# Optimization experiments

Measured on AMD Instinct MI355X. Metric: run time of the kernel, lower is better.

Reference implementation:

```python
import jax, jax.numpy as jnp
import numpy as np

K_SIZE = 5
SIGMA_IMG = 0.2
SIGMA_VGG = 0.02
BN_EPS = 1e-5
NORM = 2.0  # 2 * len(GPU_IDS), assuming 1 device


def _window_shifts(x, k):
    # x: (n, C, H, W) -> (n, C, H, W, k*k) neighbor values for every offset in
    # the k x k window, zero-padded at image borders.
    r = k // 2
    n, C, H, W = x.shape
    xp = jnp.pad(x, ((0, 0), (0, 0), (r, r), (r, r)))
    cols = [xp[:, :, di:di + H, dj:dj + W] for di in range(k) for dj in range(k)]
    return jnp.stack(cols, axis=-1)


def _modularity(img, seg, k, sigma):
    # img: (n, C, H, W) feature map; seg: (n, K, H, W) soft assignments.
    n, K, H, W = seg.shape
    seg2 = _window_shifts(seg, k)                                  # (n,K,H,W,kk)
    img2 = _window_shifts(img, k)                                  # (n,C,H,W,kk)
    valid = _window_shifts(jnp.ones((1, 1, H, W), img.dtype), k)[:, 0]  # (1,H,W,kk)
    d2 = ((img[..., None] - img2) ** 2).sum(axis=1)                # (n,H,W,kk)
    w12 = jax.lax.stop_gradient(jnp.exp(-d2 / (2.0 * sigma * sigma)) * valid)
    # numerator: sum over pixels & pairs of p1*p2*w12, per (n, K)
    num = jnp.einsum('nkhw,nkhwp,nhwp->nk', seg, seg2, w12)
    # p1 (sum over pairs of p1/n_pairs) == seg; w1 = sum over pairs of w12
    w1 = w12.sum(axis=-1)                                          # (n,H,W)
    den = jnp.einsum('nhw,nkhw->nk', w1, seg)
    rel = num / den                                                # (n,K)
    return rel.sum(axis=1) / (K * n)                               # (n,)


def _conv(x, w, b):
    y = jax.lax.conv_general_dilated(x, w, (1, 1), 'SAME',
                                     dimension_numbers=('NCHW', 'OIHW', 'NCHW'))
    return y + b[None, :, None, None]


def _maxpool2(x):
    return jax.lax.reduce_window(x, -jnp.inf, jax.lax.max,
                                 (1, 1, 2, 2), (1, 1, 2, 2), 'VALID')


def _avgpool2(x):
    n, c, h, w = x.shape
    return x.reshape(n, c, h // 2, 2, w // 2, 2).mean(axis=(3, 5))


def _vgg8(x, w1, b1, w2, b2, w3, b3, w4, b4):
    # VGG16 features[:8]: conv1_1, conv1_2, maxpool, conv2_1, conv2_2 (relu each)
    x = jax.nn.relu(_conv(x, w1, b1))
    x = jax.nn.relu(_conv(x, w2, b2))
    x = _maxpool2(x)
    x = jax.nn.relu(_conv(x, w3, b3))
    x = jax.nn.relu(_conv(x, w4, b4))
    return x


def _batchnorm(x):
    # fresh BatchNorm2d in training mode (weight=1, bias=0), then detach
    m = x.mean(axis=(0, 2, 3), keepdims=True)
    v = x.var(axis=(0, 2, 3), keepdims=True)
    return jax.lax.stop_gradient((x - m) / jnp.sqrt(v + BN_EPS))


def setup_inputs() -> dict:
    key = jax.random.key(0)
    ks = jax.random.split(key, 6)
    images = jax.random.uniform(ks[0], (4, 3, 128, 128), jnp.float32)
    seg = jax.random.uniform(ks[1], (4, 8, 128, 128), jnp.float32)
    segmentation = seg / seg.sum(axis=1, keepdims=True)
    w1 = jax.random.normal(ks[2], (64, 3, 3, 3), jnp.float32) * 0.1
    w2 = jax.random.normal(ks[3], (64, 64, 3, 3), jnp.float32) * 0.05
    w3 = jax.random.normal(ks[4], (128, 64, 3, 3), jnp.float32) * 0.05
    w4 = jax.random.normal(ks[5], (128, 128, 3, 3), jnp.float32) * 0.03
    return {'images': images, 'segmentation': segmentation,
            'w1': w1, 'b1': jnp.zeros(64), 'w2': w2, 'b2': jnp.zeros(64),
            'w3': w3, 'b3': jnp.zeros(128), 'w4': w4, 'b4': jnp.zeros(128)}


def reference(images, segmentation, w1, b1, w2, b2, w3, b3, w4, b4):
    fich = _batchnorm(_vgg8(images, w1, b1, w2, b2, w3, b3, w4, b4))  # (n,128,64,64)
    images_n = _batchnorm(images)
    down_seg = segmentation
    while down_seg.shape[-1] != fich.shape[-1]:
        down_seg = _avgpool2(down_seg)
    loss = (_modularity(fich, down_seg, K_SIZE, SIGMA_VGG).sum()
            + _modularity(images_n, segmentation, K_SIZE, SIGMA_IMG).sum())
    return loss / NORM
```

## Files before the change

kernel.cpp:

```cpp
#include <hip/hip_runtime.h>
#include <hip/hip_bf16.h>
#include <math.h>

typedef __attribute__((ext_vector_type(8))) short short8;
typedef __attribute__((ext_vector_type(4))) float floatx4;
typedef unsigned short ushortT;

__device__ inline short f2bf(float v) {
    __hip_bfloat16 h = __float2bfloat16(v);
    union { __hip_bfloat16 h; short s; } u; u.h = h; return u.s;
}

#define OFF_C2    0
#define OFF_PAD4  8388608
#define OFF_FICH  12849152
#define OFF_PAD2  21237760
#define OFF_PAD3  29890560
#define OFF_WP2   32120832
#define OFF_WP3   32194560
#define OFF_WP4   32342016
#define OFF_ST    33947648
#define OFF_P64   33951744
#define OFF_P128  33968128
#define OFF_PBN   34033664
#define OFF_PIMG  34295808

__global__ __launch_bounds__(256) void prologue(
    char* ws, const float* __restrict__ images,
    const float* __restrict__ w1, const float* __restrict__ b1,
    const float* __restrict__ w2, const float* __restrict__ w3,
    const float* __restrict__ w4)
{
    __shared__ float plds[3 * 720];
    __shared__ float rs[256], rs2[256];

    int b = blockIdx.x;
    int tid = threadIdx.x;

    if (b >= 1362) {
        int bid = b - 1362;
        int txt = bid & 7; bid >>= 3;
        int tyt = bid & 7; bid >>= 3;
        int ocg = bid & 7; bid >>= 3;
        int n = bid;
        int x0 = txt * 16, y0 = tyt * 16;
        int tx = tid & 15, ty = tid >> 4;
        short* outp = (short*)(ws + OFF_PAD2);

        for (int i = tid; i < 972; i += 256) {
            int cc = i / 324; int rem = i - cc * 324;
            int r = rem / 18, c = rem - r * 18;
            int y = y0 - 1 + r, x = x0 - 1 + c;
            float v = 0.f;
            if ((unsigned)y < 128u && (unsigned)x < 128u)
                v = images[((size_t)(n * 3 + cc) * 128 + y) * 128 + x];
            plds[cc * 720 + r * 40 + c] = v;
        }
        __syncthreads();

        float acc[8];
#pragma unroll
        for (int oc = 0; oc < 8; ++oc) acc[oc] = 0.f;
        const float* w_g = w1 + (size_t)(ocg * 8) * 27;
#pragma unroll
        for (int cc = 0; cc < 3; ++cc) {
            const float* base = &plds[cc * 720 + ty * 40 + tx];
            float i00 = base[0],  i01 = base[1],  i02 = base[2];
            float i10 = base[40], i11 = base[41], i12 = base[42];
            float i20 = base[80], i21 = base[81], i22 = base[82];
            const float* wp = w_g + cc * 9;
#pragma unroll
            for (int oc = 0; oc < 8; ++oc) {
                const float* wq = wp + oc * 27;
                float a = acc[oc];
                a = fmaf(wq[0], i00, a); a = fmaf(wq[1], i01, a); a = fmaf(wq[2], i02, a);
                a = fmaf(wq[3], i10, a); a = fmaf(wq[4], i11, a); a = fmaf(wq[5], i12, a);
                a = fmaf(wq[6], i20, a); a = fmaf(wq[7], i21, a); a = fmaf(wq[8], i22, a);
                acc[oc] = a;
            }
        }
        int oy = y0 + ty, ox = x0 + tx;
        short* o = outp + ((size_t)(n * 130 + oy + 1) * 130 + ox + 1) * 64 + ocg * 8;
#pragma unroll
        for (int oc = 0; oc < 8; ++oc) {
            float v = fmaxf(acc[oc] + b1[ocg * 8 + oc], 0.f);
            o[oc] = f2bf(v);
        }
        return;
    }

    if (b < 162) {
        int t = b * 256 + tid;
        short* base; int Hp, Wp, C; int idx;
        if (t < 16512)      { base = (short*)(ws + OFF_PAD2); Hp = 130; Wp = 130; C = 64;  idx = t; }
        else if (t < 24832) { base = (short*)(ws + OFF_PAD3); Hp = 66;  Wp = 66;  C = 64;  idx = t - 16512; }
        else if (t < 41472) { base = (short*)(ws + OFF_PAD4); Hp = 66;  Wp = 66;  C = 128; idx = t - 24832; }
        else return;
        int c8 = idx % (C / 8); int rest = idx / (C / 8);
        int haloPx = 2 * Wp + 2 * (Hp - 2);
        int p = rest % haloPx; int n = rest / haloPx;
        int y, x;
        if (p < Wp)          { y = 0;      x = p; }
        else if (p < 2 * Wp) { y = Hp - 1; x = p - Wp; }
        else { int j = p - 2 * Wp; y = 1 + (j >> 1); x = (j & 1) ? (Wp - 1) : 0; }
        short8 z = {0, 0, 0, 0, 0, 0, 0, 0};
        *(short8*)&base[((size_t)((n * Hp + y) * Wp) + x) * C + c8 * 8] = z;
        return;
    }
    if (b < 1170) {
        int e = (b - 162) * 256 + tid;
        const float* w; short* wp; int CIN, NTALL;
        if (e < 36864)       { w = w2; wp = (short*)(ws + OFF_WP2); CIN = 64;  NTALL = 4; }
        else if (e < 110592) { e -= 36864;  w = w3; wp = (short*)(ws + OFF_WP3); CIN = 64;  NTALL = 8; }
        else if (e < 258048) { e -= 110592; w = w4; wp = (short*)(ws + OFF_WP4); CIN = 128; NTALL = 8; }
        else return;
        int j = e & 7; int L = (e >> 3) & 63; int rest = e >> 9;
        int nt = rest % NTALL; int rest2 = rest / NTALL;
        int KT = CIN / 32;
        int kt = rest2 % KT; int t = rest2 / KT;
        int oc = nt * 16 + (L & 15);
        int ci = kt * 32 + (L >> 4) * 8 + j;
        wp[e] = f2bf(w[((size_t)oc * CIN + ci) * 9 + t]);
        return;
    }
    {
        float* part = (float*)(ws + OFF_PIMG);
        int bb = b - 1170;
        int c = bb >> 6, chunk = bb & 63;
        int base = chunk * 1024 + tid;
        float s = 0.f, s2 = 0.f;
#pragma unroll
        for (int k = 0; k < 4; ++k) {
            int i = base + k * 256;
            int n = i >> 14, hw = i & 16383;
            float v = images[(((size_t)(n * 3 + c)) << 14) + hw];
            s += v; s2 = fmaf(v, v, s2);
        }
        rs[tid] = s; rs2[tid] = s2;
        __syncthreads();
        for (int k = 128; k > 0; k >>= 1) {
            if (tid < k) { rs[tid] += rs[tid + k]; rs2[tid] += rs2[tid + k]; }
            __syncthreads();
        }
        if (tid == 0) { part[bb * 2] = rs[0]; part[bb * 2 + 1] = rs2[0]; }
    }
}

__global__ __launch_bounds__(256) void conv2_pool(
    const short* __restrict__ inp,
    const short* __restrict__ wp,
    const float* __restrict__ bias,
    short* __restrict__ outp)
{
    constexpr int CIN = 64;
    constexpr int Hp = 130, Wp = 130;

    int bid = blockIdx.x;
    int o2 = bid & 1; bid >>= 1;
    int xt = bid & 1; bid >>= 1;
    int yq = bid & 31; bid >>= 5;
    int n = bid;
    int y0 = yq * 4;
    int x0 = xt * 64;

    int tid = threadIdx.x;
    int wv = tid >> 6, lane = tid & 63;
    int lm = lane & 15, q = lane >> 4;
    int px0 = x0 + 16 * wv;
    int ntb = o2 * 2;

    floatx4 acc[4][2];
#pragma unroll
    for (int d = 0; d < 4; ++d)
#pragma unroll
        for (int t = 0; t < 2; ++t) acc[d][t] = (floatx4){0.f, 0.f, 0.f, 0.f};

    const short* a_m = inp + lm * CIN + q * 8;
    const short* wbase = wp + ((size_t)ntb * 64 + lane) * 8;

    for (int kt = 0; kt < 2; ++kt) {
        int kofs = kt * 32;
#pragma unroll
        for (int s = 0; s < 3; ++s) {
            const short* acol = a_m + ((size_t)((n * Hp + y0) * Wp) + px0 + s) * CIN + kofs;
            short8 av[6];
#pragma unroll
            for (int j = 0; j < 6; ++j)
                av[j] = *(const short8*)(acol + (size_t)j * Wp * CIN);
#pragma unroll
            for (int r = 0; r < 3; ++r) {
                const short* bp = wbase + (size_t)(((r * 3 + s) * 2 + kt) * 4) * 512;
                short8 b0 = *(const short8*)bp;
                short8 b1 = *(const short8*)(bp + 512);
#pragma unroll
                for (int d = 0; d < 4; ++d) {
                    acc[d][0] = __builtin_amdgcn_mfma_f32_16x16x32_bf16(av[r + d], b0, acc[d][0], 0, 0, 0);
                    acc[d][1] = __builtin_amdgcn_mfma_f32_16x16x32_bf16(av[r + d], b1, acc[d][1], 0, 0, 0);
                }
            }
        }
    }

    int ox = (px0 + q * 4) >> 1;
#pragma unroll
    for (int t2 = 0; t2 < 2; ++t2) {
        int oc = (ntb + t2) * 16 + lm;
        float bs = bias[oc];
#pragma unroll
        for (int p = 0; p < 2; ++p) {
            float v00 = fmaxf(acc[2 * p][t2][0] + bs, 0.f);
            float v01 = fmaxf(acc[2 * p][t2][1] + bs, 0.f);
            float v02 = fmaxf(acc[2 * p][t2][2] + bs, 0.f);
            float v03 = fmaxf(acc[2 * p][t2][3] + bs, 0.f);
            float v10 = fmaxf(acc[2 * p + 1][t2][0] + bs, 0.f);
            float v11 = fmaxf(acc[2 * p + 1][t2][1] + bs, 0.f);
            float v12 = fmaxf(acc[2 * p + 1][t2][2] + bs, 0.f);
            float v13 = fmaxf(acc[2 * p + 1][t2][3] + bs, 0.f);
            float m0 = fmaxf(fmaxf(v00, v01), fmaxf(v10, v11));
            float m1 = fmaxf(fmaxf(v02, v03), fmaxf(v12, v13));
            int oy = yq * 2 + p;
            short* o = outp + ((size_t)(n * 66 + oy + 1) * 66 + ox + 1) * 64 + oc;
            o[0]  = f2bf(m0);
            o[64] = f2bf(m1);
        }
    }
}

__device__ __forceinline__ void mod128_body(
    int obid,
    const float* __restrict__ img, const float* __restrict__ pimg,
    const float* __restrict__ seg, float* __restrict__ part,
    float (*il)[12][4], float (*sl)[12][14], float* stm)
{
    int t = threadIdx.x;
    int w = t >> 6, lane = t & 63;
    int tx = lane & 7, ty = lane >> 3;

    if (t < 64) {
#pragma unroll
        for (int ch = 0; ch < 3; ++ch) {
            float s  = pimg[(ch * 64 + t) * 2];
            float s2 = pimg[(ch * 64 + t) * 2 + 1];
#pragma unroll
            for (int sh = 32; sh > 0; sh >>= 1) {
                s += __shfl_xor(s, sh, 64);
                s2 += __shfl_xor(s2, sh, 64);
            }
            if (t == 0) {
                float mean = s * (1.f / 65536.f);
                float var = s2 * (1.f / 65536.f) - mean * mean;
                stm[ch] = mean;
                stm[3 + ch] = 1.f / sqrtf(var + 1e-5f);
            }
        }
    }

    int bid = obid;
    int bx = bid & 15; bid >>= 4;
    int by = bid & 15; bid >>= 4;
    int n = bid;
    int x0 = bx * 8, y0 = by * 8;

    for (int i = t; i < 8 * 144; i += 256) {
        int k = i / 144;
        int rem = i - k * 144;
        int r = rem / 12, c = rem - r * 12;
        int y = y0 - 2 + r, x = x0 - 2 + c;
        float v = 0.f;
        if ((unsigned)y < 128u && (unsigned)x < 128u)
            v = seg[((size_t)(n * 8 + k) * 128 + y) * 128 + x];
        sl[k][r][c] = v;
    }
    __syncthreads();

    float mn0 = stm[0], mn1 = stm[1], mn2 = stm[2];
    float rs0 = stm[3], rs1 = stm[4], rs2 = stm[5];

    for (int i = t; i < 432; i += 256) {
        int ch = i / 144; int pix = i - ch * 144;
        int r = pix / 12, c = pix - r * 12;
        int y = y0 - 2 + r, x = x0 - 2 + c;
        float v = 0.f;
        if ((unsigned)y < 128u && (unsigned)x < 128u) {
            float raw = img[(((size_t)(n * 3 + ch)) << 14) + y * 128 + x];
            float mn = ch == 0 ? mn0 : (ch == 1 ? mn1 : mn2);
            float rs = ch == 0 ? rs0 : (ch == 1 ? rs1 : rs2);
            v = (raw - mn) * rs;
        }
        il[r][c][ch] = v;
    }
    __syncthreads();

    const float minus_inv2s2 = -1.0f / (2.0f * 0.2f * 0.2f);
    float c0 = il[ty + 2][tx + 2][0];
    float c1 = il[ty + 2][tx + 2][1];
    float c2 = il[ty + 2][tx + 2][2];

    float wgt[25];
    float w1 = 0.f;
#pragma unroll
    for (int di = 0; di < 5; ++di)
#pragma unroll
        for (int dj = 0; dj < 5; ++dj) {
            int y2 = y0 + ty + di - 2, x2 = x0 + tx + dj - 2;
            float bias = ((unsigned)y2 < 128u && (unsigned)x2 < 128u) ? 0.f : 1e30f;
            const float* np = &il[ty + di][tx + dj][0];
            float e0 = c0 - np[0], e1 = c1 - np[1], e2 = c2 - np[2];
            float d = bias + fmaf(e2, e2, fmaf(e1, e1, e0 * e0));
            float wv = __expf(d * minus_inv2s2);
            wgt[di * 5 + dj] = wv;
            w1 += wv;
        }

#pragma unroll
    for (int kk = 0; kk < 2; ++kk) {
        int k = w * 2 + kk;
        float s = 0.f;
#pragma unroll
        for (int di = 0; di < 5; ++di)
#pragma unroll
            for (int dj = 0; dj < 5; ++dj)
                s = fmaf(wgt[di * 5 + dj], sl[k][ty + di][tx + dj], s);
        float sc = sl[k][ty + 2][tx + 2];
        float numk = s * sc;
        float denk = w1 * sc;
#pragma unroll
        for (int sft = 32; sft > 0; sft >>= 1) {
            numk += __shfl_xor(numk, sft, 64);
            denk += __shfl_xor(denk, sft, 64);
        }
        if (lane == 0) {
            part[(size_t)obid * 16 + k * 2] = numk;
            part[(size_t)obid * 16 + k * 2 + 1] = denk;
        }
    }
}

__global__ __launch_bounds__(256) void conv3_mod128(
    const short* __restrict__ inp,
    const short* __restrict__ wp,
    const float* __restrict__ bias,
    short* __restrict__ outp,
    const float* __restrict__ img,
    const float* __restrict__ pimg,
    const float* __restrict__ seg,
    float* __restrict__ p128)
{
    __shared__ float il[12][12][4];
    __shared__ float sl[8][12][14];
    __shared__ float stm[6];

    if (blockIdx.x >= 512) {
        mod128_body(blockIdx.x - 512, img, pimg, seg, p128, il, sl, stm);
        return;
    }

    constexpr int CIN = 64, COUT = 128, Hp = 66, Wp = 66, KT = 2, NTALL = 8;

    int bid = blockIdx.x;
    int bn = bid & 3; bid >>= 2;
    int yq = bid & 31; bid >>= 5;
    int n = bid;
    int y0 = yq * 2;

    int tid = threadIdx.x;
    int wv = tid >> 6, lane = tid & 63;
    int lm = lane & 15, q = lane >> 4;
    int px0 = 16 * wv;
    int ntb = bn * 2;

    floatx4 acc[2][2];
#pragma unroll
    for (int d = 0; d < 2; ++d)
#pragma unroll
        for (int t = 0; t < 2; ++t) acc[d][t] = (floatx4){0.f, 0.f, 0.f, 0.f};

    const short* a_m = inp + lm * CIN + q * 8;
    const short* wbase = wp + ((size_t)ntb * 64 + lane) * 8;

    for (int kt = 0; kt < KT; ++kt) {
        int kofs = kt * 32;
#pragma unroll
        for (int s = 0; s < 3; ++s) {
            const short* acol = a_m + ((size_t)((n * Hp + y0) * Wp) + px0 + s) * CIN + kofs;
            short8 av[4];
#pragma unroll
            for (int j = 0; j < 4; ++j)
                av[j] = *(const short8*)(acol + (size_t)j * Wp * CIN);
#pragma unroll
            for (int r = 0; r < 3; ++r) {
                const short* bp = wbase + (size_t)(((r * 3 + s) * KT + kt) * NTALL) * 512;
                short8 b0 = *(const short8*)bp;
                short8 b1 = *(const short8*)(bp + 512);
#pragma unroll
                for (int d = 0; d < 2; ++d) {
                    acc[d][0] = __builtin_amdgcn_mfma_f32_16x16x32_bf16(av[r + d], b0, acc[d][0], 0, 0, 0);
                    acc[d][1] = __builtin_amdgcn_mfma_f32_16x16x32_bf16(av[r + d], b1, acc[d][1], 0, 0, 0);
                }
            }
        }
    }

#pragma unroll
    for (int t2 = 0; t2 < 2; ++t2) {
        int oc = (ntb + t2) * 16 + lm;
        float bs = bias[oc];
#pragma unroll
        for (int d = 0; d < 2; ++d) {
#pragma unroll
            for (int i = 0; i < 4; ++i) {
                int px = px0 + q * 4 + i;
                float v = fmaxf(acc[d][t2][i] + bs, 0.f);
                outp[((size_t)(n * Hp + y0 + d + 1) * Wp + px + 1) * COUT + oc] = f2bf(v);
            }
        }
    }
}

__global__ __launch_bounds__(256) void conv4_bn(
    const short* __restrict__ inp,
    const short* __restrict__ wp,
    const float* __restrict__ bias,
    float* __restrict__ out,
    float* __restrict__ part)
{
    constexpr int CIN = 128, Hp = 66, Wp = 66, KT = 4, NTALL = 8;

    int bid = blockIdx.x;
    int bn = bid & 3; bid >>= 2;
    int yq = bid & 31; bid >>= 5;
    int n = bid;
    int y0 = yq * 2;

    int tid = threadIdx.x;
    int wv = tid >> 6, lane = tid & 63;
    int lm = lane & 15, q = lane >> 4;
    int px0 = 16 * wv;
    int ntb = bn * 2;

    floatx4 acc[2][2];
#pragma unroll
    for (int d = 0; d < 2; ++d)
#pragma unroll
        for (int t = 0; t < 2; ++t) acc[d][t] = (floatx4){0.f, 0.f, 0.f, 0.f};

    const short* a_m = inp + lm * CIN + q * 8;
    const short* wbase = wp + ((size_t)ntb * 64 + lane) * 8;

    for (int kt = 0; kt < KT; ++kt) {
        int kofs = kt * 32;
#pragma unroll
        for (int s = 0; s < 3; ++s) {
            const short* acol = a_m + ((size_t)((n * Hp + y0) * Wp) + px0 + s) * CIN + kofs;
            short8 av[4];
#pragma unroll
            for (int j = 0; j < 4; ++j)
                av[j] = *(const short8*)(acol + (size_t)j * Wp * CIN);
#pragma unroll
            for (int r = 0; r < 3; ++r) {
                const short* bp = wbase + (size_t)(((r * 3 + s) * KT + kt) * NTALL) * 512;
                short8 b0 = *(const short8*)bp;
                short8 b1 = *(const short8*)(bp + 512);
#pragma unroll
                for (int d = 0; d < 2; ++d) {
                    acc[d][0] = __builtin_amdgcn_mfma_f32_16x16x32_bf16(av[r + d], b0, acc[d][0], 0, 0, 0);
                    acc[d][1] = __builtin_amdgcn_mfma_f32_16x16x32_bf16(av[r + d], b1, acc[d][1], 0, 0, 0);
                }
            }
        }
    }

    __shared__ float ps[4][2][16], ps2[4][2][16];
#pragma unroll
    for (int t2 = 0; t2 < 2; ++t2) {
        int oc = (ntb + t2) * 16 + lm;
        float bs = bias[oc];
        float sv = 0.f, sv2 = 0.f;
#pragma unroll
        for (int d = 0; d < 2; ++d) {
#pragma unroll
            for (int i = 0; i < 4; ++i) {
                int px = px0 + q * 4 + i;
                float v = fmaxf(acc[d][t2][i] + bs, 0.f);
                out[((size_t)(n * 64 + y0 + d) * 64 + px) * 128 + oc] = v;
                sv += v; sv2 = fmaf(v, v, sv2);
            }
        }
        sv  += __shfl_xor(sv, 16, 64);  sv  += __shfl_xor(sv, 32, 64);
        sv2 += __shfl_xor(sv2, 16, 64); sv2 += __shfl_xor(sv2, 32, 64);
        if (q == 0) { ps[wv][t2][lm] = sv; ps2[wv][t2][lm] = sv2; }
    }
    __syncthreads();
    if (tid < 32) {
        int t_ = tid >> 4, lm_ = tid & 15;
        float a  = ps[0][t_][lm_] + ps[1][t_][lm_] + ps[2][t_][lm_] + ps[3][t_][lm_];
        float a2 = ps2[0][t_][lm_] + ps2[1][t_][lm_] + ps2[2][t_][lm_] + ps2[3][t_][lm_];
        part[(size_t)blockIdx.x * 64 + tid * 2]     = a;
        part[(size_t)blockIdx.x * 64 + tid * 2 + 1] = a2;
    }
}

__global__ __launch_bounds__(256) void stats_fin(const float* __restrict__ part,
                                                 float* __restrict__ st)
{
    int ch = blockIdx.x;
    int t = threadIdx.x;
    int bn = ch >> 5, lc = ch & 31;
    __shared__ float rs[128], rs2[128];
    if (t < 128) {
        const float* p = part + ((size_t)(t * 4 + bn)) * 64 + lc * 2;
        rs[t] = p[0]; rs2[t] = p[1];
    }
    __syncthreads();
    for (int k = 64; k > 0; k >>= 1) {
        if (t < k) { rs[t] += rs[t + k]; rs2[t] += rs2[t + k]; }
        __syncthreads();
    }
    if (t == 0) {
        float mean = rs[0] * (1.f / 16384.f);
        float var = rs2[0] * (1.f / 16384.f) - mean * mean;
        st[ch] = 1.f / sqrtf(var + 1e-5f);
    }
}

__global__ __launch_bounds__(256) void modularity64(
    const float* __restrict__ xt,
    const float* __restrict__ seg,
    const float* __restrict__ st,
    float* __restrict__ part)
{
    __shared__ float fl[4 * 2880];
    __shared__ float sl[8][12][14];

    int tid = threadIdx.x;
    int w = tid >> 6, lane = tid & 63;
    int tx = lane & 7, ty = lane >> 3;
    int obid = blockIdx.x;
    int bid = obid;
    int bx = bid & 7; bid >>= 3;
    int by = bid & 7; bid >>= 3;
    int n = bid;
    int x0 = bx * 8, y0 = by * 8;

    for (int i = tid; i < 8 * 144; i += 256) {
        int k = i / 144;
        int rem = i - k * 144;
        int r = rem / 12, c = rem - r * 12;
        int y = y0 - 2 + r, x = x0 - 2 + c;
        float v = 0.f;
        if ((unsigned)y < 64u && (unsigned)x < 64u) {
            const float* p = seg + ((size_t)(n * 8 + k) * 128 + 2 * y) * 128 + 2 * x;
            float2 a = *(const float2*)p;
            float2 b = *(const float2*)(p + 128);
            v = 0.25f * ((a.x + a.y) + (b.x + b.y));
        }
        sl[k][r][c] = v;
    }

    float* slab = fl + w * 2880;

    float d2p[25];
#pragma unroll
    for (int di = 0; di < 5; ++di)
#pragma unroll
        for (int dj = 0; dj < 5; ++dj) {
            int y2 = y0 + ty + di - 2, x2 = x0 + tx + dj - 2;
            float bias = ((unsigned)y2 < 64u && (unsigned)x2 < 64u) ? 0.f : 1e30f;
            d2p[di * 5 + dj] = (w == 0) ? bias : 0.f;
        }

    for (int r8 = 0; r8 < 2; ++r8) {
        int ch0 = w * 32 + r8 * 16;
        for (int i = lane; i < 576; i += 64) {
            int pix = i >> 2, q = i & 3;
            int r = pix / 12, c = pix - r * 12;
            int y = y0 - 2 + r, x = x0 - 2 + c;
            float4 v = make_float4(0.f, 0.f, 0.f, 0.f);
            if ((unsigned)y < 64u && (unsigned)x < 64u) {
                v = *(const float4*)&xt[((size_t)((n * 64 + y) * 64 + x)) * 128 + ch0 + q * 4];
                float4 sv = *(const float4*)&st[ch0 + q * 4];
                v.x *= sv.x; v.y *= sv.y; v.z *= sv.z; v.w *= sv.w;
            }
            *(float4*)&slab[(r * 12 + c) * 20 + q * 4] = v;
        }

        const float* ctr = &slab[((ty + 2) * 12 + tx + 2) * 20];
        float4 c0 = *(const float4*)(ctr + 0);
        float4 c1 = *(const float4*)(ctr + 4);
        float4 c2 = *(const float4*)(ctr + 8);
        float4 c3 = *(const float4*)(ctr + 12);
#pragma unroll
        for (int di = 0; di < 5; ++di)
#pragma unroll
            for (int dj = 0; dj < 5; ++dj) {
                const float* np = &slab[((ty + di) * 12 + tx + dj) * 20];
                float4 v0 = *(const float4*)(np + 0);
                float4 v1 = *(const float4*)(np + 4);
                float4 v2 = *(const float4*)(np + 8);
                float4 v3 = *(const float4*)(np + 12);
                float d = d2p[di * 5 + dj];
                float e;
                e = c0.x - v0.x; d = fmaf(e, e, d);
                e = c0.y - v0.y; d = fmaf(e, e, d);
                e = c0.z - v0.z; d = fmaf(e, e, d);
                e = c0.w - v0.w; d = fmaf(e, e, d);
                e = c1.x - v1.x; d = fmaf(e, e, d);
                e = c1.y - v1.y; d = fmaf(e, e, d);
                e = c1.z - v1.z; d = fmaf(e, e, d);
                e = c1.w - v1.w; d = fmaf(e, e, d);
                e = c2.x - v2.x; d = fmaf(e, e, d);
                e = c2.y - v2.y; d = fmaf(e, e, d);
                e = c2.z - v2.z; d = fmaf(e, e, d);
                e = c2.w - v2.w; d = fmaf(e, e, d);
                e = c3.x - v3.x; d = fmaf(e, e, d);
                e = c3.y - v3.y; d = fmaf(e, e, d);
                e = c3.z - v3.z; d = fmaf(e, e, d);
                e = c3.w - v3.w; d = fmaf(e, e, d);
                d2p[di * 5 + dj] = d;
            }
    }

#pragma unroll
    for (int j = 0; j < 25; ++j) slab[lane * 25 + j] = d2p[j];
    __syncthreads();

    const float minus_inv2s2 = -1.0f / (2.0f * 0.02f * 0.02f);
    for (int i = tid; i < 1600; i += 256) {
        float d = fl[i] + fl[2880 + i] + fl[5760 + i] + fl[8640 + i];
        fl[i] = expf(d * minus_inv2s2);
    }
    __syncthreads();

    float wgt[25];
    float w1 = 0.f;
#pragma unroll
    for (int j = 0; j < 25; ++j) { wgt[j] = fl[lane * 25 + j]; w1 += wgt[j]; }
#pragma unroll
    for (int kk = 0; kk < 2; ++kk) {
        int k = w * 2 + kk;
        float s = 0.f;
#pragma unroll
        for (int di = 0; di < 5; ++di)
#pragma unroll
            for (int dj = 0; dj < 5; ++dj)
                s = fmaf(wgt[di * 5 + dj], sl[k][ty + di][tx + dj], s);
        float sc = sl[k][ty + 2][tx + 2];
        float numk = s * sc;
        float denk = w1 * sc;
#pragma unroll
        for (int sh = 32; sh > 0; sh >>= 1) {
            numk += __shfl_xor(numk, sh, 64);
            denk += __shfl_xor(denk, sh, 64);
        }
        if (lane == 0) {
            part[(size_t)obid * 16 + k * 2] = numk;
            part[(size_t)obid * 16 + k * 2 + 1] = denk;
        }
    }
}

__global__ __launch_bounds__(1024) void reduce_finalize(
    const float* __restrict__ p64, const float* __restrict__ p128,
    float* __restrict__ out)
{
    int t = threadIdx.x;
    int j = t >> 4, s = t & 15;
    float num = 0.f, den = 0.f;
    if (j < 32) {
        int n = j >> 3, k = j & 7;
#pragma unroll
        for (int i = 0; i < 4; ++i) {
            int b = s * 4 + i;
            const float* p = p64 + ((size_t)(n * 64 + b)) * 16 + k * 2;
            num += p[0]; den += p[1];
        }
    } else {
        int jj = j - 32; int n = jj >> 3, k = jj & 7;
#pragma unroll
        for (int i = 0; i < 16; ++i) {
            int b = s * 16 + i;
            const float* p = p128 + ((size_t)(n * 256 + b)) * 16 + k * 2;
            num += p[0]; den += p[1];
        }
    }
#pragma unroll
    for (int sh = 8; sh > 0; sh >>= 1) {
        num += __shfl_xor(num, sh, 16);
        den += __shfl_xor(den, sh, 16);
    }
    __shared__ float rn[64], rd[64];
    if (s == 0) { rn[j] = num; rd[j] = den; }
    __syncthreads();
    if (t < 64) {
        float v = rn[t] / rd[t];
#pragma unroll
        for (int sh = 32; sh > 0; sh >>= 1) v += __shfl_xor(v, sh, 64);
        if (t == 0) out[0] = v * (1.0f / 64.0f);
    }
}

extern "C" void kernel_launch(void* const* d_in, const int* in_sizes, int n_in,
                              void* d_out, int out_size, void* d_ws, size_t ws_size,
                              hipStream_t stream)
{
    const float* images = (const float*)d_in[0];
    const float* seg    = (const float*)d_in[1];
    const float* w1 = (const float*)d_in[2]; const float* b1 = (const float*)d_in[3];
    const float* w2 = (const float*)d_in[4]; const float* b2 = (const float*)d_in[5];
    const float* w3 = (const float*)d_in[6]; const float* b3 = (const float*)d_in[7];
    const float* w4 = (const float*)d_in[8]; const float* b4 = (const float*)d_in[9];
    float* out = (float*)d_out;
    char* ws = (char*)d_ws;
    short* PAD2 = (short*)(ws + OFF_PAD2);
    short* PAD3 = (short*)(ws + OFF_PAD3);
    short* PAD4 = (short*)(ws + OFF_PAD4);
    float* FICH = (float*)(ws + OFF_FICH);
    short* WP2  = (short*)(ws + OFF_WP2);
    short* WP3  = (short*)(ws + OFF_WP3);
    short* WP4  = (short*)(ws + OFF_WP4);
    float* ST   = (float*)(ws + OFF_ST);
    float* P64  = (float*)(ws + OFF_P64);
    float* P128 = (float*)(ws + OFF_P128);
    float* PBN  = (float*)(ws + OFF_PBN);
    float* PIMG = (float*)(ws + OFF_PIMG);

    prologue<<<3410, 256, 0, stream>>>(ws, images, w1, b1, w2, w3, w4);
    conv2_pool<<<512, 256, 0, stream>>>(PAD2, WP2, b2, PAD3);
    conv3_mod128<<<1536, 256, 0, stream>>>(PAD3, WP3, b3, PAD4,
                                           images, PIMG, seg, P128);
    conv4_bn<<<512, 256, 0, stream>>>(PAD4, WP4, b4, FICH, PBN);
    stats_fin<<<128, 256, 0, stream>>>(PBN, ST);
    modularity64<<<256, 256, 0, stream>>>(FICH, seg, ST, P64);
    reduce_finalize<<<1, 1024, 0, stream>>>(P64, P128, out);
}
```

Measured before the change: 162.6 us.

## Widen conv1 blocks to 32 channels and move mod128 tail into mod64 launch

Conv1 blocks in the prologue now compute 32 output channels per thread instead of 8, with 4-wide packed bf16 stores. This reduces block count and redundant input tile loads. Half of the image-modularity blocks (512 of 1024) are moved out of the conv3 kernel into a combined launch with the feature-map modularity kernel, so the small 256-block mod64 launch fills the GPU better and conv3 is shorter. The cost is higher register pressure from the 32 accumulators, which may reduce occupancy.

```diff
diff --git a/kernel.cpp b/kernel.cpp
--- a/kernel.cpp
+++ b/kernel.cpp
@@ -3,6 +3,7 @@
 #include <math.h>
 
 typedef __attribute__((ext_vector_type(8))) short short8;
+typedef __attribute__((ext_vector_type(4))) short short4v;
 typedef __attribute__((ext_vector_type(4))) float floatx4;
 typedef unsigned short ushortT;
 
@@ -41,7 +42,7 @@
         int bid = b - 1362;
         int txt = bid & 7; bid >>= 3;
         int tyt = bid & 7; bid >>= 3;
-        int ocg = bid & 7; bid >>= 3;
+        int og = bid & 1; bid >>= 1;
         int n = bid;
         int x0 = txt * 16, y0 = tyt * 16;
         int tx = tid & 15, ty = tid >> 4;
@@ -58,20 +59,19 @@
         }
         __syncthreads();
 
-        float acc[8];
-#pragma unroll
-        for (int oc = 0; oc < 8; ++oc) acc[oc] = 0.f;
-        const float* w_g = w1 + (size_t)(ocg * 8) * 27;
+        float acc[32];
+#pragma unroll
+        for (int oc = 0; oc < 32; ++oc) acc[oc] = 0.f;
+        const float* w_g = w1 + (size_t)(og * 32) * 27;
 #pragma unroll
         for (int cc = 0; cc < 3; ++cc) {
             const float* base = &plds[cc * 720 + ty * 40 + tx];
             float i00 = base[0],  i01 = base[1],  i02 = base[2];
             float i10 = base[40], i11 = base[41], i12 = base[42];
             float i20 = base[80], i21 = base[81], i22 = base[82];
-            const float* wp = w_g + cc * 9;
-#pragma unroll
-            for (int oc = 0; oc < 8; ++oc) {
-                const float* wq = wp + oc * 27;
+#pragma unroll
+            for (int oc = 0; oc < 32; ++oc) {
+                const float* wq = w_g + oc * 27 + cc * 9;
                 float a = acc[oc];
                 a = fmaf(wq[0], i00, a); a = fmaf(wq[1], i01, a); a = fmaf(wq[2], i02, a);
                 a = fmaf(wq[3], i10, a); a = fmaf(wq[4], i11, a); a = fmaf(wq[5], i12, a);
@@ -80,11 +80,17 @@
             }
         }
         int oy = y0 + ty, ox = x0 + tx;
-        short* o = outp + ((size_t)(n * 130 + oy + 1) * 130 + ox + 1) * 64 + ocg * 8;
-#pragma unroll
-        for (int oc = 0; oc < 8; ++oc) {
-            float v = fmaxf(acc[oc] + b1[ocg * 8 + oc], 0.f);
-            o[oc] = f2bf(v);
+        short* o = outp + ((size_t)(n * 130 + oy + 1) * 130 + ox + 1) * 64 + og * 32;
+#pragma unroll
+        for (int g = 0; g < 8; ++g) {
+            short4v pk;
+#pragma unroll
+            for (int j = 0; j < 4; ++j) {
+                int oc = g * 4 + j;
+                float v = fmaxf(acc[oc] + b1[og * 32 + oc], 0.f);
+                pk[j] = f2bf(v);
+            }
+            *(short4v*)&o[g * 4] = pk;
         }
         return;
     }
@@ -523,19 +529,15 @@
     }
 }
 
-__global__ __launch_bounds__(256) void modularity64(
-    const float* __restrict__ xt,
-    const float* __restrict__ seg,
-    const float* __restrict__ st,
-    float* __restrict__ part)
-{
-    __shared__ float fl[4 * 2880];
-    __shared__ float sl[8][12][14];
-
+__device__ __forceinline__ void mod64_body(
+    int obid,
+    const float* __restrict__ xt, const float* __restrict__ seg,
+    const float* __restrict__ st, float* __restrict__ part,
+    float* fl, float (*sl)[12][14])
+{
     int tid = threadIdx.x;
     int w = tid >> 6, lane = tid & 63;
     int tx = lane & 7, ty = lane >> 3;
-    int obid = blockIdx.x;
     int bid = obid;
     int bx = bid & 7; bid >>= 3;
     int by = bid & 7; bid >>= 3;
@@ -659,6 +661,27 @@
     }
 }
 
+__global__ __launch_bounds__(256) void mod64_all(
+    const float* __restrict__ xt,
+    const float* __restrict__ seg,
+    const float* __restrict__ st,
+    const float* __restrict__ img,
+    const float* __restrict__ pimg,
+    float* __restrict__ p64, float* __restrict__ p128)
+{
+    __shared__ float fl[4 * 2880];
+    __shared__ float sl[8][12][14];
+    __shared__ float stm[6];
+
+    int bid = blockIdx.x;
+    if (bid < 256) {
+        mod64_body(bid, xt, seg, st, p64, fl, sl);
+    } else {
+        mod128_body(512 + (bid - 256), img, pimg, seg, p128,
+                    (float(*)[12][4])fl, sl, stm);
+    }
+}
+
 __global__ __launch_bounds__(1024) void reduce_finalize(
     const float* __restrict__ p64, const float* __restrict__ p128,
     float* __restrict__ out)
@@ -724,12 +747,12 @@
     float* PBN  = (float*)(ws + OFF_PBN);
     float* PIMG = (float*)(ws + OFF_PIMG);
 
-    prologue<<<3410, 256, 0, stream>>>(ws, images, w1, b1, w2, w3, w4);
+    prologue<<<1874, 256, 0, stream>>>(ws, images, w1, b1, w2, w3, w4);
     conv2_pool<<<512, 256, 0, stream>>>(PAD2, WP2, b2, PAD3);
-    conv3_mod128<<<1536, 256, 0, stream>>>(PAD3, WP3, b3, PAD4,
+    conv3_mod128<<<1024, 256, 0, stream>>>(PAD3, WP3, b3, PAD4,
                                            images, PIMG, seg, P128);
     conv4_bn<<<512, 256, 0, stream>>>(PAD4, WP4, b4, FICH, PBN);
     stats_fin<<<128, 256, 0, stream>>>(PBN, ST);
-    modularity64<<<256, 256, 0, stream>>>(FICH, seg, ST, P64);
+    mod64_all<<<768, 256, 0, stream>>>(FICH, seg, ST, images, PIMG, P64, P128);
     reduce_finalize<<<1, 1024, 0, stream>>>(P64, P128, out);
 }
```

Result: slower. 167.5 us (+3.0%).
